# Performance work log

Measured on AMD Instinct MI355X. Metric: run time of the kernel, lower is better.

Reference implementation:

```python
import jax, jax.numpy as jnp
import numpy as np

N_BLOCKS = 96
N = N_BLOCKS ** 2          # number of image blocks = n_blocks^2
D = 1024                   # feature dim (fixed by Linear(1024+1, 128))
EPS_COS = 1e-6             # eps of F.cosine_similarity
EPS_BN = 1e-5              # BatchNorm1d eps


def setup_inputs() -> dict:
    key = jax.random.key(0)
    ks = jax.random.split(key, 6)
    return {
        "features": jax.random.normal(ks[0], (N, D), dtype=jnp.float32),
        "scores": jax.random.uniform(ks[1], (N,), dtype=jnp.float32),
        "W1": jax.random.normal(ks[2], (D + 1, 128), dtype=jnp.float32) * 0.03,
        "b1": jnp.zeros((128,), jnp.float32),
        "g1": jnp.ones((128,), jnp.float32),
        "be1": jnp.zeros((128,), jnp.float32),
        "W2": jax.random.normal(ks[3], (128, 64), dtype=jnp.float32) * 0.08,
        "b2": jnp.zeros((64,), jnp.float32),
        "g2": jnp.ones((64,), jnp.float32),
        "be2": jnp.zeros((64,), jnp.float32),
        "W3": jax.random.normal(ks[4], (64, 1), dtype=jnp.float32) * 0.12,
        "b3": jnp.zeros((1,), jnp.float32),
    }


def _gaussian_similarity(features):
    # Vectorized form of the O(N^2) pairwise loop:
    #   cos_ij = <f_i, f_j> / max(|f_i||f_j|, eps)
    #   sigma^2 = D * (0.5 + 0.5 * cos)  ->  2*sigma^2 = D * (1 + cos)
    #   sim_ij = exp(-|f_i - f_j|^2 / (2*sigma^2)),  sim_ii = 1
    sq = jnp.sum(features * features, axis=-1)          # [N] squared norms
    gram = features @ features.T                          # [N, N] big GEMM
    norms = jnp.sqrt(sq)
    cos = gram / jnp.maximum(norms[:, None] * norms[None, :], EPS_COS)
    d2 = jnp.maximum(sq[:, None] + sq[None, :] - 2.0 * gram, 0.0)
    denom = jnp.maximum(jnp.float32(D) * (1.0 + cos), EPS_COS)
    sim = jnp.exp(-d2 / denom)
    eye = jnp.eye(sim.shape[0], dtype=bool)
    return jnp.where(eye, jnp.float32(1.0), sim)


def _bn_eval(h, gamma, beta):
    # BatchNorm1d in eval mode with init running stats (mean=0, var=1).
    return gamma * (h / jnp.sqrt(1.0 + EPS_BN)) + beta


def reference(features, scores, W1, b1, g1, be1, W2, b2, g2, be2, W3, b3):
    sim = _gaussian_similarity(features)                  # [N, N]
    x = jnp.concatenate([features, scores[:, None]], axis=1)  # [N, D+1]
    h = jax.nn.relu(_bn_eval(x @ W1 + b1, g1, be1))       # [N, 128]
    h = jax.nn.relu(_bn_eval(h @ W2 + b2, g2, be2))       # [N, 64]
    agg = jax.nn.sigmoid(h @ W3 + b3)[:, 0]               # [N]
    sim_mean = jnp.mean(sim, axis=1)                      # [N]
    # Torch broadcast [N,1] * [N] -> [N,N], then .mean() == mean(agg)*mean(sim_mean)
    return jnp.mean(agg) * jnp.mean(sim_mean)


if __name__ == "__main__":
    out = reference(**setup_inputs())
    print(out)
```

## Files before the change

### kernel.cpp

```cpp
#include <hip/hip_runtime.h>

#define N_IMG 9216
#define DFEAT 1024
#define NBR 72
#define NPAIR 1332

typedef __attribute__((ext_vector_type(8))) short short8;
typedef __attribute__((ext_vector_type(4))) float floatx4;
typedef __attribute__((ext_vector_type(16))) float floatx16;
typedef __attribute__((ext_vector_type(4))) int intx4;
typedef __attribute__((ext_vector_type(8))) int intx8;

#define C1F 0.0014088818759657845f
#define C2F 0.05308355472172724f

__device__ __forceinline__ void async_copy16(const void* g, void* l) {
  __builtin_amdgcn_global_load_lds((const __attribute__((address_space(1))) void*)g,
                                   (__attribute__((address_space(3))) void*)l,
                                   16, 0, 0);
}

__device__ __forceinline__ unsigned short f2bf(float x) {
  union { float f; unsigned u; } a; a.f = x;
  unsigned u = a.u;
  u += 0x7fffu + ((u >> 16) & 1u);
  return (unsigned short)(u >> 16);
}

__device__ __forceinline__ unsigned q4(float z) {
  unsigned sg = (__float_as_uint(z) >> 28) & 8u;
  float a = fabsf(z);
  unsigned c = (a < 0.25f) ? 0u : (a < 0.75f) ? 1u : (a < 1.25f) ? 2u :
               (a < 1.75f) ? 3u : (a < 2.5f)  ? 4u : (a < 3.5f)  ? 5u :
               (a < 5.0f)  ? 6u : 7u;
  return c | sg;
}
__device__ __forceinline__ unsigned short pk4(float4 v, float sc) {
  unsigned b0 = q4(v.x * sc) | (q4(v.y * sc) << 4);
  unsigned b1 = q4(v.z * sc) | (q4(v.w * sc) << 4);
  return (unsigned short)(b0 | (b1 << 8));
}

__device__ __forceinline__ intx8 ext8(intx4 v) {
  intx8 r;
  r[0] = v[0]; r[1] = v[1]; r[2] = v[2]; r[3] = v[3];
  r[4] = 0; r[5] = 0; r[6] = 0; r[7] = 0;
  return r;
}

__global__ __launch_bounds__(256) void convert_prep(const float* __restrict__ f,
                                                    const float* __restrict__ W1,
                                                    unsigned char* __restrict__ fbT,
                                                    float* __restrict__ sL,
                                                    float* __restrict__ pL,
                                                    unsigned short* __restrict__ W1t,
                                                    double* __restrict__ sums) {
  int b = blockIdx.x, t = threadIdx.x;
  if (b < 2304) {
    int lane = t & 63, wave = t >> 6;
    int row = b * 4 + wave;
    const float4* src = (const float4*)f + (size_t)row * 256;
    float4 v0 = src[lane], v1 = src[64 + lane], v2 = src[128 + lane], v3 = src[192 + lane];
    float s = v0.x * v0.x + v0.y * v0.y + v0.z * v0.z + v0.w * v0.w
            + v1.x * v1.x + v1.y * v1.y + v1.z * v1.z + v1.w * v1.w
            + v2.x * v2.x + v2.y * v2.y + v2.z * v2.z + v2.w * v2.w
            + v3.x * v3.x + v3.y * v3.y + v3.z * v3.z + v3.w * v3.w;
#pragma unroll
    for (int off = 32; off > 0; off >>= 1) s += __shfl_xor(s, off, 64);
    float zsc = rsqrtf(s) * 32.f;
    unsigned short u0 = pk4(v0, zsc), u1 = pk4(v1, zsc),
                   u2 = pk4(v2, zsc), u3 = pk4(v3, zsc);
    unsigned char* tb = fbT + (size_t)(row >> 5) * 16384 + (row & 31) * 32 + (lane & 15) * 2;
    int ko = (lane >> 4) * 1024;
    *(unsigned short*)(tb + ko) = u0;
    *(unsigned short*)(tb + ko + 4096) = u1;
    *(unsigned short*)(tb + ko + 8192) = u2;
    *(unsigned short*)(tb + ko + 12288) = u3;
    if (lane == 0) {
      sL[row] = s * C1F;
      pL[row] = sqrtf(s) * C2F;
    }
  } else {
    int j = b - 2304;
    if (j == 0 && t < 2) sums[t] = 0.0;
    for (int k = t; k < DFEAT; k += 256)
      W1t[(size_t)j * DFEAT + k] = f2bf(W1[(size_t)k * 128 + j]);
  }
}

__global__ __launch_bounds__(256, 2) void gram_sim(const unsigned char* __restrict__ fbT,
                                                   const float* __restrict__ sL,
                                                   const float* __restrict__ pL,
                                                   double* __restrict__ sums) {
  int x = blockIdx.x & 7, ii = blockIdx.x >> 3;
  int L = (x < 4) ? x * 167 + ii : 668 + (x - 4) * 166 + ii;
  int rem = L, bcol = 0;
  for (;;) {
    int mlim = 2 * bcol + 2; if (mlim > NBR) mlim = NBR;
    if (rem < mlim) break;
    rem -= mlim; bcol++;
  }
  int brow = rem;

  __shared__ float sA[128], pA[128], sB[256], pB[256];
  __shared__ float wpart[4];

  int t = threadIdx.x, lane = t & 63, wave = t >> 6;
  if (t < 128) { sA[t] = sL[brow * 128 + t]; pA[t] = pL[brow * 128 + t]; }
  sB[t] = sL[bcol * 256 + t];
  pB[t] = pL[bcol * 256 + t];
  __syncthreads();

  const int wr = (wave & 1) * 64, wc = (wave >> 1) * 128;
  const int r32 = lane & 31, kh = lane >> 5;
  const int loff = r32 * 32 + kh * 16;

  const unsigned char* pa0 = fbT + (size_t)(brow * 4 + (wr >> 5)) * 16384 + loff;
  const unsigned char* pa1 = pa0 + 16384;
  const unsigned char* pb0 = fbT + (size_t)(bcol * 8 + (wc >> 5)) * 16384 + loff;
  const unsigned char* pb1 = pb0 + 16384;
  const unsigned char* pb2 = pb0 + 32768;
  const unsigned char* pb3 = pb0 + 49152;

  floatx16 acc[2][4];
#pragma unroll
  for (int mi = 0; mi < 2; mi++)
#pragma unroll
    for (int ni = 0; ni < 4; ni++)
#pragma unroll
      for (int e = 0; e < 16; e++) acc[mi][ni][e] = 0.f;

  intx4 bA[3][2], bB[3][4];
#define LDSET(s, kb)                                                        \
  {                                                                         \
    const int o = (kb) * 1024;                                              \
    bA[s][0] = *(const intx4*)(pa0 + o); bA[s][1] = *(const intx4*)(pa1 + o); \
    bB[s][0] = *(const intx4*)(pb0 + o); bB[s][1] = *(const intx4*)(pb1 + o); \
    bB[s][2] = *(const intx4*)(pb2 + o); bB[s][3] = *(const intx4*)(pb3 + o); \
  }
  LDSET(0, 0)
  LDSET(1, 1)
#pragma unroll
  for (int kb = 0; kb < 16; kb++) {
    const int cur = kb % 3, nxt = (kb + 2) % 3;
    if (kb < 14) LDSET(nxt, kb + 2)
    intx8 A8[2], B8[4];
#pragma unroll
    for (int mi = 0; mi < 2; mi++) A8[mi] = ext8(bA[cur][mi]);
#pragma unroll
    for (int ni = 0; ni < 4; ni++) B8[ni] = ext8(bB[cur][ni]);
#pragma unroll
    for (int mi = 0; mi < 2; mi++)
#pragma unroll
      for (int ni = 0; ni < 4; ni++)
        acc[mi][ni] = __builtin_amdgcn_mfma_scale_f32_32x32x64_f8f6f4(
            A8[mi], B8[ni], acc[mi][ni], 4, 4,
            0, 0x7F7F7F7F, 0, 0x7F7F7F7F);
  }
#undef LDSET

  const bool interior = (brow < 2 * bcol);
  float lsum = 0.f;
#pragma unroll
  for (int ni = 0; ni < 4; ni++) {
    int j_loc = wc + ni * 32 + r32;
    float sj = sB[j_loc], pj = pB[j_loc];
    int j_g = bcol * 256 + j_loc;
#pragma unroll
    for (int mi = 0; mi < 2; mi++) {
      int rbase = wr + mi * 32 + 4 * kh;
#pragma unroll
      for (int reg = 0; reg < 16; reg++) {
        int i_loc = rbase + (reg & 3) + 8 * (reg >> 2);
        float g = acc[mi][ni][reg];
        float si = sA[i_loc], pi = pA[i_loc];
        float r = __builtin_amdgcn_rcpf(1024.f + g);
        float del = pi * pj;
        float gam = si + sj + del;
        float tt = gam * r;
        float sim = __builtin_amdgcn_exp2f(fmaf(-1024.f, tt, del));
        if (interior) {
          lsum += sim;
        } else {
          int i_g = brow * 128 + i_loc;
          lsum += (i_g < j_g) ? 2.f * sim : (i_g == j_g ? 1.f : 0.f);
        }
      }
    }
  }
  if (interior) lsum *= 2.f;
#pragma unroll
  for (int off = 32; off > 0; off >>= 1) lsum += __shfl_down(lsum, off, 64);
  if (lane == 0) wpart[wave] = lsum;
  __syncthreads();
  if (t == 0)
    atomicAdd(&sums[0], (double)(wpart[0] + wpart[1] + wpart[2] + wpart[3]));
}

__global__ __launch_bounds__(256) void mlp_full(const float* __restrict__ f,
                                                const unsigned short* __restrict__ W1t,
                                                const float* __restrict__ scores,
                                                const float* __restrict__ W1,
                                                const float* __restrict__ b1,
                                                const float* __restrict__ g1,
                                                const float* __restrict__ be1,
                                                const float* __restrict__ W2, const float* __restrict__ b2,
                                                const float* __restrict__ g2, const float* __restrict__ be2,
                                                const float* __restrict__ W3, const float* __restrict__ b3,
                                                double* __restrict__ sums) {
  int r0 = blockIdx.x * 32;

  __shared__ __align__(16) float As32[32 * 64];
  __shared__ __align__(16) unsigned short Bs[128 * 64];
  __shared__ float h1s[32][128];
  __shared__ float h2s[32][65];
  __shared__ float sc[32], b1s[128], g1s[128], be1s[128], wls[128], ls[32];

  int t = threadIdx.x, lane = t & 63, wave = t >> 6;
  if (t < 32) sc[t] = scores[r0 + t];
  if (t < 128) {
    b1s[t] = b1[t]; g1s[t] = g1[t]; be1s[t] = be1[t];
    wls[t] = W1[(size_t)DFEAT * 128 + t];
  }

  floatx4 acc[4];
#pragma unroll
  for (int b = 0; b < 4; b++) acc[b] = (floatx4){0.f, 0.f, 0.f, 0.f};

  const int wr = (wave & 1) * 16, wc = (wave >> 1) * 64;

  for (int k0 = 0; k0 < DFEAT; k0 += 64) {
    __syncthreads();
    {
      int c = t, rA = c >> 4, p = c & 15, l = p ^ (rA & 15);
      async_copy16(f + (size_t)(r0 + rA) * DFEAT + k0 + l * 4, (char*)As32 + c * 16);
      c = t + 256; rA = c >> 4; p = c & 15; l = p ^ (rA & 15);
      async_copy16(f + (size_t)(r0 + rA) * DFEAT + k0 + l * 4, (char*)As32 + c * 16);
#pragma unroll
      for (int q = 0; q < 4; q++) {
        int cc = t + q * 256, rB = cc >> 3, pp = cc & 7, ll = pp ^ (rB & 7);
        async_copy16(W1t + (size_t)rB * DFEAT + k0 + ll * 8, (char*)Bs + cc * 16);
      }
    }
    __syncthreads();

    const int mrow = lane & 15;
#pragma unroll
    for (int ks = 0; ks < 2; ks++) {
      const int kq = ks * 32 + (lane >> 4) * 8;
      short8 a, b[4];
      {
        int row = wr + mrow;
        int l0 = kq >> 2;
        int p0 = l0 ^ (row & 15), p1 = (l0 + 1) ^ (row & 15);
        float4 f0 = *(const float4*)&As32[row * 64 + p0 * 4];
        float4 f1 = *(const float4*)&As32[row * 64 + p1 * 4];
        a[0] = (short)f2bf(f0.x); a[1] = (short)f2bf(f0.y);
        a[2] = (short)f2bf(f0.z); a[3] = (short)f2bf(f0.w);
        a[4] = (short)f2bf(f1.x); a[5] = (short)f2bf(f1.y);
        a[6] = (short)f2bf(f1.z); a[7] = (short)f2bf(f1.w);
      }
#pragma unroll
      for (int nt = 0; nt < 4; nt++) {
        int row = wc + nt * 16 + mrow;
        int p = (kq >> 3) ^ (row & 7);
        b[nt] = *(const short8*)&Bs[row * 64 + p * 8];
      }
#pragma unroll
      for (int nt = 0; nt < 4; nt++)
        acc[nt] = __builtin_amdgcn_mfma_f32_16x16x32_bf16(a, b[nt], acc[nt], 0, 0, 0);
    }
  }

  const float inv = 1.0f / sqrtf(1.0f + 1e-5f);
  const int rq = (lane >> 4) * 4, cn = lane & 15;
#pragma unroll
  for (int nt = 0; nt < 4; nt++) {
    int j = wc + nt * 16 + cn;
    float bj = b1s[j], gj = g1s[j] * inv, bej = be1s[j], wj = wls[j];
#pragma unroll
    for (int rr = 0; rr < 4; rr++) {
      int iL = wr + rq + rr;
      float pre = acc[nt][rr] + sc[iL] * wj + bj;
      h1s[iL][j] = fmaxf(gj * pre + bej, 0.f);
    }
  }
  __syncthreads();

  {
    int j = t & 63, rg = (t >> 6) * 8;
    float a2[8];
#pragma unroll
    for (int rr = 0; rr < 8; rr++) a2[rr] = 0.f;
    for (int k = 0; k < 128; k++) {
      float w = W2[k * 64 + j];
#pragma unroll
      for (int rr = 0; rr < 8; rr++) a2[rr] = fmaf(h1s[rg + rr][k], w, a2[rr]);
    }
    float scv = g2[j] * inv, bi = b2[j], be = be2[j];
#pragma unroll
    for (int rr = 0; rr < 8; rr++)
      h2s[rg + rr][j] = fmaxf(scv * (a2[rr] + bi) + be, 0.f);
  }
  __syncthreads();

  if (t < 32) {
    float z = b3[0];
#pragma unroll
    for (int k = 0; k < 64; k++) z = fmaf(h2s[t][k], W3[k], z);
    ls[t] = 1.f / (1.f + __expf(-z));
  }
  __syncthreads();
  if (t == 0) {
    float s = 0.f;
#pragma unroll
    for (int iL = 0; iL < 32; iL++) s += ls[iL];
    atomicAdd(&sums[1], (double)s);
  }
}

__global__ void finalize(const double* __restrict__ sums, float* __restrict__ out) {
  double simmean = sums[0] / ((double)N_IMG * (double)N_IMG);
  double aggmean = sums[1] / (double)N_IMG;
  out[0] = (float)(aggmean * simmean);
}

extern "C" void kernel_launch(void* const* d_in, const int* in_sizes, int n_in,
                              void* d_out, int out_size, void* d_ws, size_t ws_size,
                              hipStream_t stream) {
  const float* f      = (const float*)d_in[0];
  const float* scores = (const float*)d_in[1];
  const float* W1 = (const float*)d_in[2];
  const float* b1 = (const float*)d_in[3];
  const float* g1 = (const float*)d_in[4];
  const float* be1 = (const float*)d_in[5];
  const float* W2 = (const float*)d_in[6];
  const float* b2 = (const float*)d_in[7];
  const float* g2 = (const float*)d_in[8];
  const float* be2 = (const float*)d_in[9];
  const float* W3 = (const float*)d_in[10];
  const float* b3 = (const float*)d_in[11];

  char* ws = (char*)d_ws;
  unsigned char* fbT  = (unsigned char*)ws;
  float* sL           = (float*)(ws + 4718592);
  float* pL           = (float*)(ws + 4755456);
  unsigned short* W1t = (unsigned short*)(ws + 4792320);
  double* sums        = (double*)(ws + 5054464);

  convert_prep<<<2432, 256, 0, stream>>>(f, W1, fbT, sL, pL, W1t, sums);
  gram_sim<<<NPAIR, 256, 0, stream>>>(fbT, sL, pL, sums);
  mlp_full<<<288, 256, 0, stream>>>(f, W1t, scores, W1, b1, g1, be1,
                                    W2, b2, g2, be2, W3, b3, sums);
  finalize<<<1, 1, 0, stream>>>(sums, (float*)d_out);
}
```

Before: 182.3 us.

## Fuse gram-similarity, MLP and finalize into one heterogeneous kernel launch

Merges the gram_sim and mlp_full kernels into a single grid where the first 288 blocks run the MLP and the rest run the similarity tiles, sharing one dynamically partitioned shared-memory buffer. The finalize kernel is replaced by a last-block-done atomic counter, and the counter is reset in convert_prep. This removes two launches and lets the two independent workloads overlap on the GPU. In exchange the fused kernel carries the larger shared-memory footprint and the register demand of both paths, which may lower occupancy for the gram tiles.

Measured after the change: 207.2 us. 1.14x slower.

```diff
diff --git a/kernel.cpp b/kernel.cpp
--- a/kernel.cpp
+++ b/kernel.cpp
@@ -4,6 +4,8 @@
 #define DFEAT 1024
 #define NBR 72
 #define NPAIR 1332
+#define MLPB 288
+#define NGRID (NPAIR + MLPB)
 
 typedef __attribute__((ext_vector_type(8))) short short8;
 typedef __attribute__((ext_vector_type(4))) float floatx4;
@@ -54,7 +56,8 @@
                                                     float* __restrict__ sL,
                                                     float* __restrict__ pL,
                                                     unsigned short* __restrict__ W1t,
-                                                    double* __restrict__ sums) {
+                                                    double* __restrict__ sums,
+                                                    unsigned* __restrict__ ctr) {
   int b = blockIdx.x, t = threadIdx.x;
   if (b < 2304) {
     int lane = t & 63, wave = t >> 6;
@@ -82,247 +85,261 @@
     }
   } else {
     int j = b - 2304;
-    if (j == 0 && t < 2) sums[t] = 0.0;
+    if (j == 0) {
+      if (t < 2) sums[t] = 0.0;
+      if (t == 2) *ctr = 0u;
+    }
     for (int k = t; k < DFEAT; k += 256)
       W1t[(size_t)j * DFEAT + k] = f2bf(W1[(size_t)k * 128 + j]);
   }
 }
 
-__global__ __launch_bounds__(256, 2) void gram_sim(const unsigned char* __restrict__ fbT,
-                                                   const float* __restrict__ sL,
-                                                   const float* __restrict__ pL,
-                                                   double* __restrict__ sums) {
-  int x = blockIdx.x & 7, ii = blockIdx.x >> 3;
-  int L = (x < 4) ? x * 167 + ii : 668 + (x - 4) * 166 + ii;
-  int rem = L, bcol = 0;
-  for (;;) {
-    int mlim = 2 * bcol + 2; if (mlim > NBR) mlim = NBR;
-    if (rem < mlim) break;
-    rem -= mlim; bcol++;
+__global__ __launch_bounds__(256, 2) void fused_main(
+    const unsigned char* __restrict__ fbT, const float* __restrict__ sL,
+    const float* __restrict__ pL, const float* __restrict__ f,
+    const unsigned short* __restrict__ W1t, const float* __restrict__ scores,
+    const float* __restrict__ W1, const float* __restrict__ b1,
+    const float* __restrict__ g1, const float* __restrict__ be1,
+    const float* __restrict__ W2, const float* __restrict__ b2,
+    const float* __restrict__ g2, const float* __restrict__ be2,
+    const float* __restrict__ W3, const float* __restrict__ b3,
+    double* __restrict__ sums, unsigned* __restrict__ ctr,
+    float* __restrict__ out) {
+  __shared__ __align__(16) char smem[51584];
+  int bid = blockIdx.x, t = threadIdx.x, lane = t & 63, wave = t >> 6;
+
+  if (bid < MLPB) {
+    int r0 = bid * 32;
+    float* As32 = (float*)smem;
+    unsigned short* Bs = (unsigned short*)(smem + 8192);
+    float (*h1s)[128] = (float (*)[128])(smem + 24576);
+    float (*h2s)[65]  = (float (*)[65])(smem + 40960);
+    float* sc   = (float*)(smem + 49280);
+    float* b1s  = (float*)(smem + 49408);
+    float* g1s  = (float*)(smem + 49920);
+    float* be1s = (float*)(smem + 50432);
+    float* wls  = (float*)(smem + 50944);
+    float* ls   = (float*)(smem + 51456);
+
+    if (t < 32) sc[t] = scores[r0 + t];
+    if (t < 128) {
+      b1s[t] = b1[t]; g1s[t] = g1[t]; be1s[t] = be1[t];
+      wls[t] = W1[(size_t)DFEAT * 128 + t];
+    }
+
+    floatx4 acc[4];
+#pragma unroll
+    for (int b = 0; b < 4; b++) acc[b] = (floatx4){0.f, 0.f, 0.f, 0.f};
+
+    const int wr = (wave & 1) * 16, wc = (wave >> 1) * 64;
+
+    for (int k0 = 0; k0 < DFEAT; k0 += 64) {
+      __syncthreads();
+      {
+        int c = t, rA = c >> 4, p = c & 15, l = p ^ (rA & 15);
+        async_copy16(f + (size_t)(r0 + rA) * DFEAT + k0 + l * 4, (char*)As32 + c * 16);
+        c = t + 256; rA = c >> 4; p = c & 15; l = p ^ (rA & 15);
+        async_copy16(f + (size_t)(r0 + rA) * DFEAT + k0 + l * 4, (char*)As32 + c * 16);
+#pragma unroll
+        for (int q = 0; q < 4; q++) {
+          int cc = t + q * 256, rB = cc >> 3, pp = cc & 7, ll = pp ^ (rB & 7);
+          async_copy16(W1t + (size_t)rB * DFEAT + k0 + ll * 8, (char*)Bs + cc * 16);
+        }
+      }
+      __syncthreads();
+
+      const int mrow = lane & 15;
+#pragma unroll
+      for (int ks = 0; ks < 2; ks++) {
+        const int kq = ks * 32 + (lane >> 4) * 8;
+        short8 a, b[4];
+        {
+          int row = wr + mrow;
+          int l0 = kq >> 2;
+          int p0 = l0 ^ (row & 15), p1 = (l0 + 1) ^ (row & 15);
+          float4 f0 = *(const float4*)&As32[row * 64 + p0 * 4];
+          float4 f1 = *(const float4*)&As32[row * 64 + p1 * 4];
+          a[0] = (short)f2bf(f0.x); a[1] = (short)f2bf(f0.y);
+          a[2] = (short)f2bf(f0.z); a[3] = (short)f2bf(f0.w);
+          a[4] = (short)f2bf(f1.x); a[5] = (short)f2bf(f1.y);
+          a[6] = (short)f2bf(f1.z); a[7] = (short)f2bf(f1.w);
+        }
+#pragma unroll
+        for (int nt = 0; nt < 4; nt++) {
+          int row = wc + nt * 16 + mrow;
+          int p = (kq >> 3) ^ (row & 7);
+          b[nt] = *(const short8*)&Bs[row * 64 + p * 8];
+        }
+#pragma unroll
+        for (int nt = 0; nt < 4; nt++)
+          acc[nt] = __builtin_amdgcn_mfma_f32_16x16x32_bf16(a, b[nt], acc[nt], 0, 0, 0);
+      }
+    }
+
+    const float inv = 1.0f / sqrtf(1.0f + 1e-5f);
+    const int rq = (lane >> 4) * 4, cn = lane & 15;
+#pragma unroll
+    for (int nt = 0; nt < 4; nt++) {
+      int j = wc + nt * 16 + cn;
+      float bj = b1s[j], gj = g1s[j] * inv, bej = be1s[j], wj = wls[j];
+#pragma unroll
+      for (int rr = 0; rr < 4; rr++) {
+        int iL = wr + rq + rr;
+        float pre = acc[nt][rr] + sc[iL] * wj + bj;
+        h1s[iL][j] = fmaxf(gj * pre + bej, 0.f);
+      }
+    }
+    __syncthreads();
+
+    {
+      int j = t & 63, rg = (t >> 6) * 8;
+      float a2[8];
+#pragma unroll
+      for (int rr = 0; rr < 8; rr++) a2[rr] = 0.f;
+      for (int k = 0; k < 128; k++) {
+        float w = W2[k * 64 + j];
+#pragma unroll
+        for (int rr = 0; rr < 8; rr++) a2[rr] = fmaf(h1s[rg + rr][k], w, a2[rr]);
+      }
+      float scv = g2[j] * inv, bi = b2[j], be = be2[j];
+#pragma unroll
+      for (int rr = 0; rr < 8; rr++)
+        h2s[rg + rr][j] = fmaxf(scv * (a2[rr] + bi) + be, 0.f);
+    }
+    __syncthreads();
+
+    if (t < 32) {
+      float z = b3[0];
+#pragma unroll
+      for (int k = 0; k < 64; k++) z = fmaf(h2s[t][k], W3[k], z);
+      ls[t] = 1.f / (1.f + __expf(-z));
+    }
+    __syncthreads();
+    if (t == 0) {
+      float s = 0.f;
+#pragma unroll
+      for (int iL = 0; iL < 32; iL++) s += ls[iL];
+      atomicAdd(&sums[1], (double)s);
+    }
+  } else {
+    int gb = bid - MLPB;
+    int x = gb & 7, ii = gb >> 3;
+    int L = (x < 4) ? x * 167 + ii : 668 + (x - 4) * 166 + ii;
+    int rem = L, bcol = 0;
+    for (;;) {
+      int mlim = 2 * bcol + 2; if (mlim > NBR) mlim = NBR;
+      if (rem < mlim) break;
+      rem -= mlim; bcol++;
+    }
+    int brow = rem;
+
+    float* sA = (float*)smem;
+    float* pA = (float*)(smem + 512);
+    float* sB = (float*)(smem + 1024);
+    float* pB = (float*)(smem + 2048);
+    float* wpart = (float*)(smem + 3072);
+
+    if (t < 128) { sA[t] = sL[brow * 128 + t]; pA[t] = pL[brow * 128 + t]; }
+    sB[t] = sL[bcol * 256 + t];
+    pB[t] = pL[bcol * 256 + t];
+    __syncthreads();
+
+    const int wr = (wave & 1) * 64, wc = (wave >> 1) * 128;
+    const int r32 = lane & 31, kh = lane >> 5;
+    const int loff = r32 * 32 + kh * 16;
+
+    const unsigned char* pa0 = fbT + (size_t)(brow * 4 + (wr >> 5)) * 16384 + loff;
+    const unsigned char* pa1 = pa0 + 16384;
+    const unsigned char* pb0 = fbT + (size_t)(bcol * 8 + (wc >> 5)) * 16384 + loff;
+    const unsigned char* pb1 = pb0 + 16384;
+    const unsigned char* pb2 = pb0 + 32768;
+    const unsigned char* pb3 = pb0 + 49152;
+
+    floatx16 acc[2][4];
+#pragma unroll
+    for (int mi = 0; mi < 2; mi++)
+#pragma unroll
+      for (int ni = 0; ni < 4; ni++)
+#pragma unroll
+        for (int e = 0; e < 16; e++) acc[mi][ni][e] = 0.f;
+
+    intx4 bA[3][2], bB[3][4];
+#define LDSET(s, kb)                                                          \
+    {                                                                         \
+      const int o = (kb) * 1024;                                              \
+      bA[s][0] = *(const intx4*)(pa0 + o); bA[s][1] = *(const intx4*)(pa1 + o); \
+      bB[s][0] = *(const intx4*)(pb0 + o); bB[s][1] = *(const intx4*)(pb1 + o); \
+      bB[s][2] = *(const intx4*)(pb2 + o); bB[s][3] = *(const intx4*)(pb3 + o); \
+    }
+    LDSET(0, 0)
+    LDSET(1, 1)
+#pragma unroll
+    for (int kb = 0; kb < 16; kb++) {
+      const int cur = kb % 3, nxt = (kb + 2) % 3;
+      if (kb < 14) LDSET(nxt, kb + 2)
+      intx8 A8[2], B8[4];
+#pragma unroll
+      for (int mi = 0; mi < 2; mi++) A8[mi] = ext8(bA[cur][mi]);
+#pragma unroll
+      for (int ni = 0; ni < 4; ni++) B8[ni] = ext8(bB[cur][ni]);
+#pragma unroll
+      for (int mi = 0; mi < 2; mi++)
+#pragma unroll
+        for (int ni = 0; ni < 4; ni++)
+          acc[mi][ni] = __builtin_amdgcn_mfma_scale_f32_32x32x64_f8f6f4(
+              A8[mi], B8[ni], acc[mi][ni], 4, 4,
+              0, 0x7F7F7F7F, 0, 0x7F7F7F7F);
+    }
+#undef LDSET
+
+    const bool interior = (brow < 2 * bcol);
+    float lsum = 0.f;
+#pragma unroll
+    for (int ni = 0; ni < 4; ni++) {
+      int j_loc = wc + ni * 32 + r32;
+      float sj = sB[j_loc], pj = pB[j_loc];
+      int j_g = bcol * 256 + j_loc;
+#pragma unroll
+      for (int mi = 0; mi < 2; mi++) {
+        int rbase = wr + mi * 32 + 4 * kh;
+#pragma unroll
+        for (int reg = 0; reg < 16; reg++) {
+          int i_loc = rbase + (reg & 3) + 8 * (reg >> 2);
+          float g = acc[mi][ni][reg];
+          float si = sA[i_loc], pi = pA[i_loc];
+          float r = __builtin_amdgcn_rcpf(1024.f + g);
+          float del = pi * pj;
+          float gam = si + sj + del;
+          float tt = gam * r;
+          float sim = __builtin_amdgcn_exp2f(fmaf(-1024.f, tt, del));
+          if (interior) {
+            lsum += sim;
+          } else {
+            int i_g = brow * 128 + i_loc;
+            lsum += (i_g < j_g) ? 2.f * sim : (i_g == j_g ? 1.f : 0.f);
+          }
+        }
+      }
+    }
+    if (interior) lsum *= 2.f;
+#pragma unroll
+    for (int off = 32; off > 0; off >>= 1) lsum += __shfl_down(lsum, off, 64);
+    if (lane == 0) wpart[wave] = lsum;
+    __syncthreads();
+    if (t == 0)
+      atomicAdd(&sums[0], (double)(wpart[0] + wpart[1] + wpart[2] + wpart[3]));
   }
-  int brow = rem;
-
-  __shared__ float sA[128], pA[128], sB[256], pB[256];
-  __shared__ float wpart[4];
-
-  int t = threadIdx.x, lane = t & 63, wave = t >> 6;
-  if (t < 128) { sA[t] = sL[brow * 128 + t]; pA[t] = pL[brow * 128 + t]; }
-  sB[t] = sL[bcol * 256 + t];
-  pB[t] = pL[bcol * 256 + t];
-  __syncthreads();
-
-  const int wr = (wave & 1) * 64, wc = (wave >> 1) * 128;
-  const int r32 = lane & 31, kh = lane >> 5;
-  const int loff = r32 * 32 + kh * 16;
-
-  const unsigned char* pa0 = fbT + (size_t)(brow * 4 + (wr >> 5)) * 16384 + loff;
-  const unsigned char* pa1 = pa0 + 16384;
-  const unsigned char* pb0 = fbT + (size_t)(bcol * 8 + (wc >> 5)) * 16384 + loff;
-  const unsigned char* pb1 = pb0 + 16384;
-  const unsigned char* pb2 = pb0 + 32768;
-  const unsigned char* pb3 = pb0 + 49152;
-
-  floatx16 acc[2][4];
-#pragma unroll
-  for (int mi = 0; mi < 2; mi++)
-#pragma unroll
-    for (int ni = 0; ni < 4; ni++)
-#pragma unroll
-      for (int e = 0; e < 16; e++) acc[mi][ni][e] = 0.f;
-
-  intx4 bA[3][2], bB[3][4];
-#define LDSET(s, kb)                                                        \
-  {                                                                         \
-    const int o = (kb) * 1024;                                              \
-    bA[s][0] = *(const intx4*)(pa0 + o); bA[s][1] = *(const intx4*)(pa1 + o); \
-    bB[s][0] = *(const intx4*)(pb0 + o); bB[s][1] = *(const intx4*)(pb1 + o); \
-    bB[s][2] = *(const intx4*)(pb2 + o); bB[s][3] = *(const intx4*)(pb3 + o); \
+
+  if (t == 0) {
+    __threadfence();
+    unsigned prev = atomicAdd(ctr, 1u);
+    if (prev == (unsigned)(NGRID - 1)) {
+      __threadfence();
+      double s0 = ((volatile double*)sums)[0];
+      double s1 = ((volatile double*)sums)[1];
+      out[0] = (float)((s1 / (double)N_IMG) * (s0 / ((double)N_IMG * (double)N_IMG)));
+    }
   }
-  LDSET(0, 0)
-  LDSET(1, 1)
-#pragma unroll
-  for (int kb = 0; kb < 16; kb++) {
-    const int cur = kb % 3, nxt = (kb + 2) % 3;
-    if (kb < 14) LDSET(nxt, kb + 2)
-    intx8 A8[2], B8[4];
-#pragma unroll
-    for (int mi = 0; mi < 2; mi++) A8[mi] = ext8(bA[cur][mi]);
-#pragma unroll
-    for (int ni = 0; ni < 4; ni++) B8[ni] = ext8(bB[cur][ni]);
-#pragma unroll
-    for (int mi = 0; mi < 2; mi++)
-#pragma unroll
-      for (int ni = 0; ni < 4; ni++)
-        acc[mi][ni] = __builtin_amdgcn_mfma_scale_f32_32x32x64_f8f6f4(
-            A8[mi], B8[ni], acc[mi][ni], 4, 4,
-            0, 0x7F7F7F7F, 0, 0x7F7F7F7F);
-  }
-#undef LDSET
-
-  const bool interior = (brow < 2 * bcol);
-  float lsum = 0.f;
-#pragma unroll
-  for (int ni = 0; ni < 4; ni++) {
-    int j_loc = wc + ni * 32 + r32;
-    float sj = sB[j_loc], pj = pB[j_loc];
-    int j_g = bcol * 256 + j_loc;
-#pragma unroll
-    for (int mi = 0; mi < 2; mi++) {
-      int rbase = wr + mi * 32 + 4 * kh;
-#pragma unroll
-      for (int reg = 0; reg < 16; reg++) {
-        int i_loc = rbase + (reg & 3) + 8 * (reg >> 2);
-        float g = acc[mi][ni][reg];
-        float si = sA[i_loc], pi = pA[i_loc];
-        float r = __builtin_amdgcn_rcpf(1024.f + g);
-        float del = pi * pj;
-        float gam = si + sj + del;
-        float tt = gam * r;
-        float sim = __builtin_amdgcn_exp2f(fmaf(-1024.f, tt, del));
-        if (interior) {
-          lsum += sim;
-        } else {
-          int i_g = brow * 128 + i_loc;
-          lsum += (i_g < j_g) ? 2.f * sim : (i_g == j_g ? 1.f : 0.f);
-        }
-      }
-    }
-  }
-  if (interior) lsum *= 2.f;
-#pragma unroll
-  for (int off = 32; off > 0; off >>= 1) lsum += __shfl_down(lsum, off, 64);
-  if (lane == 0) wpart[wave] = lsum;
-  __syncthreads();
-  if (t == 0)
-    atomicAdd(&sums[0], (double)(wpart[0] + wpart[1] + wpart[2] + wpart[3]));
-}
-
-__global__ __launch_bounds__(256) void mlp_full(const float* __restrict__ f,
-                                                const unsigned short* __restrict__ W1t,
-                                                const float* __restrict__ scores,
-                                                const float* __restrict__ W1,
-                                                const float* __restrict__ b1,
-                                                const float* __restrict__ g1,
-                                                const float* __restrict__ be1,
-                                                const float* __restrict__ W2, const float* __restrict__ b2,
-                                                const float* __restrict__ g2, const float* __restrict__ be2,
-                                                const float* __restrict__ W3, const float* __restrict__ b3,
-                                                double* __restrict__ sums) {
-  int r0 = blockIdx.x * 32;
-
-  __shared__ __align__(16) float As32[32 * 64];
-  __shared__ __align__(16) unsigned short Bs[128 * 64];
-  __shared__ float h1s[32][128];
-  __shared__ float h2s[32][65];
-  __shared__ float sc[32], b1s[128], g1s[128], be1s[128], wls[128], ls[32];
-
-  int t = threadIdx.x, lane = t & 63, wave = t >> 6;
-  if (t < 32) sc[t] = scores[r0 + t];
-  if (t < 128) {
-    b1s[t] = b1[t]; g1s[t] = g1[t]; be1s[t] = be1[t];
-    wls[t] = W1[(size_t)DFEAT * 128 + t];
-  }
-
-  floatx4 acc[4];
-#pragma unroll
-  for (int b = 0; b < 4; b++) acc[b] = (floatx4){0.f, 0.f, 0.f, 0.f};
-
-  const int wr = (wave & 1) * 16, wc = (wave >> 1) * 64;
-
-  for (int k0 = 0; k0 < DFEAT; k0 += 64) {
-    __syncthreads();
-    {
-      int c = t, rA = c >> 4, p = c & 15, l = p ^ (rA & 15);
-      async_copy16(f + (size_t)(r0 + rA) * DFEAT + k0 + l * 4, (char*)As32 + c * 16);
-      c = t + 256; rA = c >> 4; p = c & 15; l = p ^ (rA & 15);
-      async_copy16(f + (size_t)(r0 + rA) * DFEAT + k0 + l * 4, (char*)As32 + c * 16);
-#pragma unroll
-      for (int q = 0; q < 4; q++) {
-        int cc = t + q * 256, rB = cc >> 3, pp = cc & 7, ll = pp ^ (rB & 7);
-        async_copy16(W1t + (size_t)rB * DFEAT + k0 + ll * 8, (char*)Bs + cc * 16);
-      }
-    }
-    __syncthreads();
-
-    const int mrow = lane & 15;
-#pragma unroll
-    for (int ks = 0; ks < 2; ks++) {
-      const int kq = ks * 32 + (lane >> 4) * 8;
-      short8 a, b[4];
-      {
-        int row = wr + mrow;
-        int l0 = kq >> 2;
-        int p0 = l0 ^ (row & 15), p1 = (l0 + 1) ^ (row & 15);
-        float4 f0 = *(const float4*)&As32[row * 64 + p0 * 4];
-        float4 f1 = *(const float4*)&As32[row * 64 + p1 * 4];
-        a[0] = (short)f2bf(f0.x); a[1] = (short)f2bf(f0.y);
-        a[2] = (short)f2bf(f0.z); a[3] = (short)f2bf(f0.w);
-        a[4] = (short)f2bf(f1.x); a[5] = (short)f2bf(f1.y);
-        a[6] = (short)f2bf(f1.z); a[7] = (short)f2bf(f1.w);
-      }
-#pragma unroll
-      for (int nt = 0; nt < 4; nt++) {
-        int row = wc + nt * 16 + mrow;
-        int p = (kq >> 3) ^ (row & 7);
-        b[nt] = *(const short8*)&Bs[row * 64 + p * 8];
-      }
-#pragma unroll
-      for (int nt = 0; nt < 4; nt++)
-        acc[nt] = __builtin_amdgcn_mfma_f32_16x16x32_bf16(a, b[nt], acc[nt], 0, 0, 0);
-    }
-  }
-
-  const float inv = 1.0f / sqrtf(1.0f + 1e-5f);
-  const int rq = (lane >> 4) * 4, cn = lane & 15;
-#pragma unroll
-  for (int nt = 0; nt < 4; nt++) {
-    int j = wc + nt * 16 + cn;
-    float bj = b1s[j], gj = g1s[j] * inv, bej = be1s[j], wj = wls[j];
-#pragma unroll
-    for (int rr = 0; rr < 4; rr++) {
-      int iL = wr + rq + rr;
-      float pre = acc[nt][rr] + sc[iL] * wj + bj;
-      h1s[iL][j] = fmaxf(gj * pre + bej, 0.f);
-    }
-  }
-  __syncthreads();
-
-  {
-    int j = t & 63, rg = (t >> 6) * 8;
-    float a2[8];
-#pragma unroll
-    for (int rr = 0; rr < 8; rr++) a2[rr] = 0.f;
-    for (int k = 0; k < 128; k++) {
-      float w = W2[k * 64 + j];
-#pragma unroll
-      for (int rr = 0; rr < 8; rr++) a2[rr] = fmaf(h1s[rg + rr][k], w, a2[rr]);
-    }
-    float scv = g2[j] * inv, bi = b2[j], be = be2[j];
-#pragma unroll
-    for (int rr = 0; rr < 8; rr++)
-      h2s[rg + rr][j] = fmaxf(scv * (a2[rr] + bi) + be, 0.f);
-  }
-  __syncthreads();
-
-  if (t < 32) {
-    float z = b3[0];
-#pragma unroll
-    for (int k = 0; k < 64; k++) z = fmaf(h2s[t][k], W3[k], z);
-    ls[t] = 1.f / (1.f + __expf(-z));
-  }
-  __syncthreads();
-  if (t == 0) {
-    float s = 0.f;
-#pragma unroll
-    for (int iL = 0; iL < 32; iL++) s += ls[iL];
-    atomicAdd(&sums[1], (double)s);
-  }
-}
-
-__global__ void finalize(const double* __restrict__ sums, float* __restrict__ out) {
-  double simmean = sums[0] / ((double)N_IMG * (double)N_IMG);
-  double aggmean = sums[1] / (double)N_IMG;
-  out[0] = (float)(aggmean * simmean);
 }
 
 extern "C" void kernel_launch(void* const* d_in, const int* in_sizes, int n_in,
@@ -347,10 +364,10 @@
   float* pL           = (float*)(ws + 4755456);
   unsigned short* W1t = (unsigned short*)(ws + 4792320);
   double* sums        = (double*)(ws + 5054464);
-
-  convert_prep<<<2432, 256, 0, stream>>>(f, W1, fbT, sL, pL, W1t, sums);
-  gram_sim<<<NPAIR, 256, 0, stream>>>(fbT, sL, pL, sums);
-  mlp_full<<<288, 256, 0, stream>>>(f, W1t, scores, W1, b1, g1, be1,
-                                    W2, b2, g2, be2, W3, b3, sums);
-  finalize<<<1, 1, 0, stream>>>(sums, (float*)d_out);
-}
+  unsigned* ctr       = (unsigned*)(ws + 5054480);
+
+  convert_prep<<<2432, 256, 0, stream>>>(f, W1, fbT, sL, pL, W1t, sums, ctr);
+  fused_main<<<NGRID, 256, 0, stream>>>(fbT, sL, pL, f, W1t, scores,
+                                        W1, b1, g1, be1, W2, b2, g2, be2, W3, b3,
+                                        sums, ctr, (float*)d_out);
+}
```

## Stage FP4 gram tiles through swizzled LDS with 256x256 blocks and fuse finalize

Applied to the files above, without the earlier changes.

The gram kernel now uses 256x256 upper-triangular tiles handled by 512-thread blocks. A and B panels are double-buffered into LDS with async global-to-LDS copies, where before each wave read directly from global memory. The feature layout gains an XOR swizzle to avoid LDS bank conflicts, and the finalize kernel is folded into the MLP kernel with a last-block atomic counter. Together these cut redundant global reads and one launch, at the cost of barriers per k-step and larger LDS use.

Result: slower. 193.6 us (+6.2%).

```diff
diff --git a/kernel.cpp b/kernel.cpp
--- a/kernel.cpp
+++ b/kernel.cpp
@@ -2,8 +2,8 @@
 
 #define N_IMG 9216
 #define DFEAT 1024
-#define NBR 72
-#define NPAIR 1332
+#define NBP 36
+#define NPAIR2 666
 
 typedef __attribute__((ext_vector_type(8))) short short8;
 typedef __attribute__((ext_vector_type(4))) float floatx4;
@@ -41,20 +41,14 @@
   return (unsigned short)(b0 | (b1 << 8));
 }
 
-__device__ __forceinline__ intx8 ext8(intx4 v) {
-  intx8 r;
-  r[0] = v[0]; r[1] = v[1]; r[2] = v[2]; r[3] = v[3];
-  r[4] = 0; r[5] = 0; r[6] = 0; r[7] = 0;
-  return r;
-}
-
 __global__ __launch_bounds__(256) void convert_prep(const float* __restrict__ f,
                                                     const float* __restrict__ W1,
                                                     unsigned char* __restrict__ fbT,
                                                     float* __restrict__ sL,
                                                     float* __restrict__ pL,
                                                     unsigned short* __restrict__ W1t,
-                                                    double* __restrict__ sums) {
+                                                    double* __restrict__ sums,
+                                                    unsigned* __restrict__ ctr) {
   int b = blockIdx.x, t = threadIdx.x;
   if (b < 2304) {
     int lane = t & 63, wave = t >> 6;
@@ -70,7 +64,10 @@
     float zsc = rsqrtf(s) * 32.f;
     unsigned short u0 = pk4(v0, zsc), u1 = pk4(v1, zsc),
                    u2 = pk4(v2, zsc), u3 = pk4(v3, zsc);
-    unsigned char* tb = fbT + (size_t)(row >> 5) * 16384 + (row & 31) * 32 + (lane & 15) * 2;
+    unsigned e = lane & 15;
+    unsigned sw = (row >> 2) & 1;
+    unsigned char* tb = fbT + (size_t)(row >> 5) * 16384 + (row & 31) * 32
+                      + (((e >> 3) ^ sw) * 16) + (e & 7) * 2;
     int ko = (lane >> 4) * 1024;
     *(unsigned short*)(tb + ko) = u0;
     *(unsigned short*)(tb + ko + 4096) = u1;
@@ -82,92 +79,110 @@
     }
   } else {
     int j = b - 2304;
-    if (j == 0 && t < 2) sums[t] = 0.0;
+    if (j == 0) {
+      if (t < 2) sums[t] = 0.0;
+      if (t == 2) *ctr = 0u;
+    }
     for (int k = t; k < DFEAT; k += 256)
       W1t[(size_t)j * DFEAT + k] = f2bf(W1[(size_t)k * 128 + j]);
   }
 }
 
-__global__ __launch_bounds__(256, 2) void gram_sim(const unsigned char* __restrict__ fbT,
+__global__ __launch_bounds__(512, 2) void gram_sim(const unsigned char* __restrict__ fbT,
                                                    const float* __restrict__ sL,
                                                    const float* __restrict__ pL,
                                                    double* __restrict__ sums) {
-  int x = blockIdx.x & 7, ii = blockIdx.x >> 3;
-  int L = (x < 4) ? x * 167 + ii : 668 + (x - 4) * 166 + ii;
+  __shared__ __align__(16) unsigned char stg[2][16384];
+  __shared__ float sA[256], pA[256], sB[256], pB[256];
+  __shared__ float wpart[8];
+
+  int bid = blockIdx.x, t = threadIdx.x, lane = t & 63, wave = t >> 6;
+  int xcd = bid & 7, t8 = bid >> 3;
+  int L = (xcd < 2 ? xcd * 84 : 168 + (xcd - 2) * 83) + t8;
   int rem = L, bcol = 0;
-  for (;;) {
-    int mlim = 2 * bcol + 2; if (mlim > NBR) mlim = NBR;
-    if (rem < mlim) break;
-    rem -= mlim; bcol++;
-  }
+  while (rem > bcol) { rem -= (bcol + 1); bcol++; }
   int brow = rem;
 
-  __shared__ float sA[128], pA[128], sB[256], pB[256];
-  __shared__ float wpart[4];
-
-  int t = threadIdx.x, lane = t & 63, wave = t >> 6;
-  if (t < 128) { sA[t] = sL[brow * 128 + t]; pA[t] = pL[brow * 128 + t]; }
-  sB[t] = sL[bcol * 256 + t];
-  pB[t] = pL[bcol * 256 + t];
-  __syncthreads();
-
-  const int wr = (wave & 1) * 64, wc = (wave >> 1) * 128;
+  if (t < 256) { sA[t] = sL[brow * 256 + t]; pA[t] = pL[brow * 256 + t]; }
+  else { int u = t & 255; sB[u] = sL[bcol * 256 + u]; pB[u] = pL[bcol * 256 + u]; }
+
+  const int spanel = (wave < 4) ? brow : bcol;
+  const int slab0 = (wave < 4) ? (2 * wave) : (2 * wave - 8);
+  const unsigned char* src0 = fbT + (size_t)(spanel * 8 + slab0) * 16384 + lane * 16;
+  const unsigned char* src1 = src0 + 16384;
+  char* dst0 = (char*)stg + wave * 2048 + lane * 16;
+
+#define STAGE(buf, kb)                                              \
+  {                                                                 \
+    async_copy16(src0 + (kb) * 1024, dst0 + (buf) * 16384);         \
+    async_copy16(src1 + (kb) * 1024, dst0 + 1024 + (buf) * 16384);  \
+  }
+
   const int r32 = lane & 31, kh = lane >> 5;
-  const int loff = r32 * 32 + kh * 16;
-
-  const unsigned char* pa0 = fbT + (size_t)(brow * 4 + (wr >> 5)) * 16384 + loff;
-  const unsigned char* pa1 = pa0 + 16384;
-  const unsigned char* pb0 = fbT + (size_t)(bcol * 8 + (wc >> 5)) * 16384 + loff;
-  const unsigned char* pb1 = pb0 + 16384;
-  const unsigned char* pb2 = pb0 + 32768;
-  const unsigned char* pb3 = pb0 + 49152;
-
-  floatx16 acc[2][4];
-#pragma unroll
-  for (int mi = 0; mi < 2; mi++)
-#pragma unroll
-    for (int ni = 0; ni < 4; ni++)
+  const int swz = (r32 >> 2) & 1;
+  const int loff = r32 * 32 + ((kh ^ swz) << 4);
+  const int wr = (wave & 1) * 128, wc = (wave >> 1) * 64;
+  const char* aBase = (const char*)stg + ((wave & 1) * 4) * 1024 + loff;
+  const char* bBase = (const char*)stg + 8192 + ((wave >> 1) * 2) * 1024 + loff;
+
+  floatx16 acc[4][2];
+#pragma unroll
+  for (int mi = 0; mi < 4; mi++)
+#pragma unroll
+    for (int ni = 0; ni < 2; ni++)
 #pragma unroll
       for (int e = 0; e < 16; e++) acc[mi][ni][e] = 0.f;
 
-  intx4 bA[3][2], bB[3][4];
-#define LDSET(s, kb)                                                        \
-  {                                                                         \
-    const int o = (kb) * 1024;                                              \
-    bA[s][0] = *(const intx4*)(pa0 + o); bA[s][1] = *(const intx4*)(pa1 + o); \
-    bB[s][0] = *(const intx4*)(pb0 + o); bB[s][1] = *(const intx4*)(pb1 + o); \
-    bB[s][2] = *(const intx4*)(pb2 + o); bB[s][3] = *(const intx4*)(pb3 + o); \
-  }
-  LDSET(0, 0)
-  LDSET(1, 1)
+  intx8 A8[4], B8[2];
+#pragma unroll
+  for (int mi = 0; mi < 4; mi++)
+#pragma unroll
+    for (int e = 0; e < 8; e++) A8[mi][e] = 0;
+#pragma unroll
+  for (int ni = 0; ni < 2; ni++)
+#pragma unroll
+    for (int e = 0; e < 8; e++) B8[ni][e] = 0;
+
+  STAGE(0, 0)
+  STAGE(1, 1)
 #pragma unroll
   for (int kb = 0; kb < 16; kb++) {
-    const int cur = kb % 3, nxt = (kb + 2) % 3;
-    if (kb < 14) LDSET(nxt, kb + 2)
-    intx8 A8[2], B8[4];
-#pragma unroll
-    for (int mi = 0; mi < 2; mi++) A8[mi] = ext8(bA[cur][mi]);
-#pragma unroll
-    for (int ni = 0; ni < 4; ni++) B8[ni] = ext8(bB[cur][ni]);
-#pragma unroll
-    for (int mi = 0; mi < 2; mi++)
-#pragma unroll
-      for (int ni = 0; ni < 4; ni++)
+    if (kb < 15) asm volatile("s_waitcnt vmcnt(2)" ::: "memory");
+    else         asm volatile("s_waitcnt vmcnt(0)" ::: "memory");
+    __builtin_amdgcn_s_barrier();
+    __builtin_amdgcn_sched_barrier(0);
+    const int cur = (kb & 1) * 16384;
+#pragma unroll
+    for (int mi = 0; mi < 4; mi++) {
+      intx4 v = *(const intx4*)(aBase + cur + mi * 1024);
+      A8[mi][0] = v[0]; A8[mi][1] = v[1]; A8[mi][2] = v[2]; A8[mi][3] = v[3];
+    }
+#pragma unroll
+    for (int ni = 0; ni < 2; ni++) {
+      intx4 v = *(const intx4*)(bBase + cur + ni * 1024);
+      B8[ni][0] = v[0]; B8[ni][1] = v[1]; B8[ni][2] = v[2]; B8[ni][3] = v[3];
+    }
+#pragma unroll
+    for (int mi = 0; mi < 4; mi++)
+#pragma unroll
+      for (int ni = 0; ni < 2; ni++)
         acc[mi][ni] = __builtin_amdgcn_mfma_scale_f32_32x32x64_f8f6f4(
             A8[mi], B8[ni], acc[mi][ni], 4, 4,
             0, 0x7F7F7F7F, 0, 0x7F7F7F7F);
-  }
-#undef LDSET
-
-  const bool interior = (brow < 2 * bcol);
+    __builtin_amdgcn_s_barrier();
+    __builtin_amdgcn_sched_barrier(0);
+    if (kb < 14) STAGE((kb & 1), kb + 2)
+  }
+#undef STAGE
+
+  const bool diag = (brow == bcol);
   float lsum = 0.f;
 #pragma unroll
-  for (int ni = 0; ni < 4; ni++) {
+  for (int ni = 0; ni < 2; ni++) {
     int j_loc = wc + ni * 32 + r32;
     float sj = sB[j_loc], pj = pB[j_loc];
-    int j_g = bcol * 256 + j_loc;
-#pragma unroll
-    for (int mi = 0; mi < 2; mi++) {
+#pragma unroll
+    for (int mi = 0; mi < 4; mi++) {
       int rbase = wr + mi * 32 + 4 * kh;
 #pragma unroll
       for (int reg = 0; reg < 16; reg++) {
@@ -177,24 +192,26 @@
         float r = __builtin_amdgcn_rcpf(1024.f + g);
         float del = pi * pj;
         float gam = si + sj + del;
-        float tt = gam * r;
-        float sim = __builtin_amdgcn_exp2f(fmaf(-1024.f, tt, del));
-        if (interior) {
+        float sim = __builtin_amdgcn_exp2f(fmaf(-1024.f, gam * r, del));
+        if (!diag) {
           lsum += sim;
         } else {
-          int i_g = brow * 128 + i_loc;
-          lsum += (i_g < j_g) ? 2.f * sim : (i_g == j_g ? 1.f : 0.f);
+          lsum += (i_loc < j_loc) ? 2.f * sim : (i_loc == j_loc ? 1.f : 0.f);
         }
       }
     }
   }
-  if (interior) lsum *= 2.f;
+  if (!diag) lsum *= 2.f;
 #pragma unroll
   for (int off = 32; off > 0; off >>= 1) lsum += __shfl_down(lsum, off, 64);
   if (lane == 0) wpart[wave] = lsum;
   __syncthreads();
-  if (t == 0)
-    atomicAdd(&sums[0], (double)(wpart[0] + wpart[1] + wpart[2] + wpart[3]));
+  if (t == 0) {
+    float bs = 0.f;
+#pragma unroll
+    for (int w = 0; w < 8; w++) bs += wpart[w];
+    atomicAdd(&sums[0], (double)bs);
+  }
 }
 
 __global__ __launch_bounds__(256) void mlp_full(const float* __restrict__ f,
@@ -207,7 +224,9 @@
                                                 const float* __restrict__ W2, const float* __restrict__ b2,
                                                 const float* __restrict__ g2, const float* __restrict__ be2,
                                                 const float* __restrict__ W3, const float* __restrict__ b3,
-                                                double* __restrict__ sums) {
+                                                double* __restrict__ sums,
+                                                unsigned* __restrict__ ctr,
+                                                float* __restrict__ out) {
   int r0 = blockIdx.x * 32;
 
   __shared__ __align__(16) float As32[32 * 64];
@@ -316,13 +335,15 @@
 #pragma unroll
     for (int iL = 0; iL < 32; iL++) s += ls[iL];
     atomicAdd(&sums[1], (double)s);
-  }
-}
-
-__global__ void finalize(const double* __restrict__ sums, float* __restrict__ out) {
-  double simmean = sums[0] / ((double)N_IMG * (double)N_IMG);
-  double aggmean = sums[1] / (double)N_IMG;
-  out[0] = (float)(aggmean * simmean);
+    __threadfence();
+    unsigned prev = atomicAdd(ctr, 1u);
+    if (prev == 287u) {
+      __threadfence();
+      double s0 = ((volatile double*)sums)[0];
+      double s1 = ((volatile double*)sums)[1];
+      out[0] = (float)((s1 / (double)N_IMG) * (s0 / ((double)N_IMG * (double)N_IMG)));
+    }
+  }
 }
 
 extern "C" void kernel_launch(void* const* d_in, const int* in_sizes, int n_in,
@@ -347,10 +368,11 @@
   float* pL           = (float*)(ws + 4755456);
   unsigned short* W1t = (unsigned short*)(ws + 4792320);
   double* sums        = (double*)(ws + 5054464);
-
-  convert_prep<<<2432, 256, 0, stream>>>(f, W1, fbT, sL, pL, W1t, sums);
-  gram_sim<<<NPAIR, 256, 0, stream>>>(fbT, sL, pL, sums);
+  unsigned* ctr       = (unsigned*)(ws + 5054480);
+
+  convert_prep<<<2432, 256, 0, stream>>>(f, W1, fbT, sL, pL, W1t, sums, ctr);
+  gram_sim<<<NPAIR2, 512, 0, stream>>>(fbT, sL, pL, sums);
   mlp_full<<<288, 256, 0, stream>>>(f, W1t, scores, W1, b1, g1, be1,
-                                    W2, b2, g2, be2, W3, b3, sums);
-  finalize<<<1, 1, 0, stream>>>(sums, (float*)d_out);
-}
+                                    W2, b2, g2, be2, W3, b3, sums, ctr,
+                                    (float*)d_out);
+}
```
